# Optimization experiments

Hardware: AMD Instinct MI355X
Metric: run time of the kernel (lower is better)

## Reference

```python
import jax, jax.numpy as jnp
import numpy as np
import math

B, S, E, H = 4, 1024, 1024, 16
HD = E // H
MAX_SEQ = 5000
THETA = 10000.0


def _freqs_cis():
    # RotaryPositionalEncoding buffer: complex64 [MAX_SEQ, E//2]
    freqs = 1.0 / (THETA ** (np.arange(0, E, 2)[: E // 2] / E))
    ang = np.outer(np.arange(MAX_SEQ), freqs)
    return jnp.asarray(np.exp(1j * ang).astype(np.complex64))


def _rope(x, idx, fc_table):
    # x: [B, S, E]; pairs consecutive channels across the FULL embed_dim
    # (applied before head splitting, faithful to the original module)
    xc = x.reshape(*x.shape[:-1], -1, 2)
    xc = jax.lax.complex(xc[..., 0], xc[..., 1])  # [B, S, E//2]
    out = xc * fc_table[idx]                       # [B, S, E//2]
    return jnp.stack([jnp.real(out), jnp.imag(out)], axis=-1).reshape(x.shape)


def reference(query, key, value, query_index, key_index, attn_mask,
              key_padding_mask, Wq, bq, Wk, bk, Wv, bv, Wo, bo):
    q = query @ Wq.T + bq
    k = key @ Wk.T + bk
    v = value @ Wv.T + bv

    fc = _freqs_cis()
    q = _rope(q, query_index, fc)
    k = _rope(k, key_index, fc)

    # torch: q = cat(q.chunk(H, dim=-1), dim=0) -> flat HEAD-MAJOR [H*B, S, HD]
    qf = q.reshape(B, S, H, HD).transpose(2, 0, 1, 3).reshape(H * B, S, HD)
    kf = k.reshape(B, S, H, HD).transpose(2, 0, 1, 3).reshape(H * B, S, HD)
    vf = v.reshape(B, S, H, HD).transpose(2, 0, 1, 3).reshape(H * B, S, HD)

    # mask: logical_or(attn_mask[Sq,Sk], kpm[B,1,Sk]) -> [B, Sq, Sk]
    m = jnp.logical_or(attn_mask[None, :, :], key_padding_mask[:, None, :])
    madd = jnp.where(m, -jnp.inf, 0.0).astype(query.dtype)
    # torch repeat_interleave(H, dim=0) yields BATCH-MAJOR flat [B*H, Sq, Sk];
    # it is added to the head-major scores as-is (faithful to the original
    # indexing, including its head/batch-order quirk)
    madd_flat = jnp.repeat(madd, H, axis=0)

    scores = jnp.einsum('nqd,nkd->nqk', qf / math.sqrt(HD), kf) + madd_flat
    w = jax.nn.softmax(scores, axis=-1)              # [H*B, Sq, Sk]
    of = jnp.einsum('nqk,nkd->nqd', w, vf)           # [H*B, Sq, HD]

    # cat(chunks(dim=0), dim=-1) -> [B, Sq, E], head-major last dim
    attn_output = of.reshape(H, B, S, HD).transpose(1, 2, 0, 3).reshape(B, S, E)
    attn_output = attn_output @ Wo.T + bo

    # stack(chunks(dim=0), dim=1).mean(1) -> [B, Sq, Sk]
    attn_weights = w.reshape(H, B, S, S).transpose(1, 0, 2, 3).mean(axis=1)
    return attn_output, attn_weights


def setup_inputs() -> dict:
    key0 = jax.random.key(0)
    ks = jax.random.split(key0, 10)
    sc = 0.02
    inp = {
        'query': jax.random.normal(ks[0], (B, S, E), jnp.float32),
        'key': jax.random.normal(ks[1], (B, S, E), jnp.float32),
        'value': jax.random.normal(ks[2], (B, S, E), jnp.float32),
        'query_index': jnp.sort(jax.random.randint(ks[3], (B, S), 0, 4096), axis=-1),
        'key_index': jnp.sort(jax.random.randint(ks[4], (B, S), 0, 4096), axis=-1),
        'attn_mask': jnp.triu(jnp.ones((S, S), jnp.bool_), k=1),  # causal
        'key_padding_mask': jnp.zeros((B, S), jnp.bool_),
        'Wq': jax.random.normal(ks[5], (E, E), jnp.float32) * sc,
        'bq': jnp.zeros((E,), jnp.float32),
        'Wk': jax.random.normal(ks[6], (E, E), jnp.float32) * sc,
        'bk': jnp.zeros((E,), jnp.float32),
        'Wv': jax.random.normal(ks[7], (E, E), jnp.float32) * sc,
        'bv': jnp.zeros((E,), jnp.float32),
        'Wo': jax.random.normal(ks[8], (E, E), jnp.float32) * sc,
        'bo': jnp.zeros((E,), jnp.float32),
    }
    return inp
```

## Files before the change

kernel.cpp:

```cpp
#include <hip/hip_runtime.h>
#include <stdint.h>
#include <math.h>

#define B_ 4
#define S_ 1024
#define E_ 1024
#define H_ 16
#define HD_ 64
#define HB_ 64

typedef __attribute__((ext_vector_type(8))) short bhalf8;
typedef __attribute__((ext_vector_type(4))) float floatx4;

__device__ __forceinline__ unsigned short f2bf(float f) {
  union { float f; unsigned u; } v; v.f = f;
  unsigned r = (v.u + 0x7FFFu + ((v.u >> 16) & 1u)) >> 16;
  return (unsigned short)r;
}
__device__ __forceinline__ float bf2f(unsigned short b) {
  union { unsigned u; float f; } v; v.u = ((unsigned)b) << 16;
  return v.f;
}
__device__ __forceinline__ unsigned short f2h(float f) {
  union { _Float16 h; unsigned short u; } v; v.h = (_Float16)f; return v.u;
}
__device__ __forceinline__ float h2f(unsigned short u) {
  union { unsigned short u; _Float16 h; } v; v.u = u; return (float)v.h;
}

__device__ __forceinline__ void gload16(const void* g, void* l) {
  __builtin_amdgcn_global_load_lds(
      (const __attribute__((address_space(1))) unsigned int*)g,
      (__attribute__((address_space(3))) unsigned int*)l, 16, 0, 0);
}

template <int NCH>
__device__ __forceinline__ void stage_tile(const unsigned short* org,
                                           unsigned short* lds, int wave, int lane) {
  const int rl = lane >> 3;
  const int scb = ((lane & 7) << 4) ^ (rl << 4);
  const char* base = (const char*)org + scb;
#pragma unroll
  for (int i = 0; i < NCH / 4; ++i) {
    const int c = wave + 4 * i;
    gload16(base + (size_t)(c * 8 + rl) * 2048, (char*)lds + c * 1024);
  }
}

__device__ __forceinline__ bhalf8 read_frag(const unsigned short* lds, int row, int kbyte) {
  const int off = row * 128 + (kbyte ^ ((row & 7) << 4));
  return *(const bhalf8*)((const char*)lds + off);
}

__global__ void detect_bool_kernel(const uint8_t* __restrict__ amask, int* __restrict__ flag) {
  if (threadIdx.x == 0 && blockIdx.x == 0) *flag = (amask[1] != 0) ? 1 : 0;
}

__global__ __launch_bounds__(256) void cvt_in_kernel(
    const float* __restrict__ q, const float* __restrict__ k,
    const float* __restrict__ v, unsigned short* __restrict__ Ab) {
  const int z = blockIdx.z;
  const float* src = (z == 0) ? q : (z == 1) ? k : v;
  unsigned short* dst = Ab + (size_t)z * 4194304;
  const size_t i = ((size_t)blockIdx.x * 256 + threadIdx.x) * 8;
  float4 a = *(const float4*)(src + i);
  float4 b = *(const float4*)(src + i + 4);
  bhalf8 r;
  r[0] = (short)f2bf(a.x); r[1] = (short)f2bf(a.y);
  r[2] = (short)f2bf(a.z); r[3] = (short)f2bf(a.w);
  r[4] = (short)f2bf(b.x); r[5] = (short)f2bf(b.y);
  r[6] = (short)f2bf(b.z); r[7] = (short)f2bf(b.w);
  *(bhalf8*)(dst + i) = r;
}

__global__ __launch_bounds__(256) void cvt_w_kernel(
    const float* __restrict__ wq, const float* __restrict__ wk,
    const float* __restrict__ wv, const float* __restrict__ wo,
    unsigned short* __restrict__ Wb) {
  const int z = blockIdx.z;
  const float* src = (z == 0) ? wq : (z == 1) ? wk : (z == 2) ? wv : wo;
  unsigned short* dst = Wb + (size_t)z * 1048576;
  const size_t i = ((size_t)blockIdx.x * 256 + threadIdx.x) * 8;
  float4 a = *(const float4*)(src + i);
  float4 b = *(const float4*)(src + i + 4);
  bhalf8 r;
  r[0] = (short)f2bf(a.x); r[1] = (short)f2bf(a.y);
  r[2] = (short)f2bf(a.z); r[3] = (short)f2bf(a.w);
  r[4] = (short)f2bf(b.x); r[5] = (short)f2bf(b.y);
  r[6] = (short)f2bf(b.z); r[7] = (short)f2bf(b.w);
  *(bhalf8*)(dst + i) = r;
}

template <bool BF16OUT>
__global__ __launch_bounds__(256) void mfma_gemm_kernel(
    const unsigned short* __restrict__ A0, const unsigned short* __restrict__ A1,
    const unsigned short* __restrict__ A2,
    const unsigned short* __restrict__ W0, const unsigned short* __restrict__ W1,
    const unsigned short* __restrict__ W2,
    const float* __restrict__ b0, const float* __restrict__ b1,
    const float* __restrict__ b2,
    void* __restrict__ C0, void* __restrict__ C1, void* __restrict__ C2) {
  const int z = blockIdx.z;
  const unsigned short* A = (z == 0) ? A0 : (z == 1) ? A1 : A2;
  const unsigned short* W = (z == 0) ? W0 : (z == 1) ? W1 : W2;
  const float* bias = (z == 0) ? b0 : (z == 1) ? b1 : b2;
  void* C = (z == 0) ? C0 : (z == 1) ? C1 : C2;
  const int lin = blockIdx.y * 8 + blockIdx.x;
  const int swz = (lin & 7) * 32 + (lin >> 3);
  const int m0 = (swz >> 3) * 128, n0 = (swz & 7) * 128;
  __shared__ unsigned short As[128 * 64];
  __shared__ unsigned short Ws[128 * 64];
  const int t = threadIdx.x, wave = t >> 6, lane = t & 63;
  const int wr = wave >> 1, wc = wave & 1;
  floatx4 acc[4][4];
  const floatx4 z4 = {0.f, 0.f, 0.f, 0.f};
#pragma unroll
  for (int i = 0; i < 4; ++i)
#pragma unroll
    for (int j = 0; j < 4; ++j) acc[i][j] = z4;

  for (int k0 = 0; k0 < 1024; k0 += 64) {
    stage_tile<16>(A + (size_t)m0 * 1024 + k0, As, wave, lane);
    stage_tile<16>(W + (size_t)n0 * 1024 + k0, Ws, wave, lane);
    __syncthreads();
#pragma unroll
    for (int ks = 0; ks < 2; ++ks) {
      const int kb = ks * 64 + ((lane >> 4) << 4);
      bhalf8 af[4], bf[4];
#pragma unroll
      for (int mi = 0; mi < 4; ++mi)
        af[mi] = read_frag(As, wr * 64 + mi * 16 + (lane & 15), kb);
#pragma unroll
      for (int ni = 0; ni < 4; ++ni)
        bf[ni] = read_frag(Ws, wc * 64 + ni * 16 + (lane & 15), kb);
#pragma unroll
      for (int mi = 0; mi < 4; ++mi)
#pragma unroll
        for (int ni = 0; ni < 4; ++ni)
          acc[mi][ni] = __builtin_amdgcn_mfma_f32_16x16x32_bf16(af[mi], bf[ni], acc[mi][ni], 0, 0, 0);
    }
    __syncthreads();
  }
#pragma unroll
  for (int mi = 0; mi < 4; ++mi)
#pragma unroll
    for (int ni = 0; ni < 4; ++ni) {
      const int col = n0 + wc * 64 + ni * 16 + (lane & 15);
      const float bv = bias[col];
#pragma unroll
      for (int r = 0; r < 4; ++r) {
        const int row = m0 + wr * 64 + mi * 16 + (lane >> 4) * 4 + r;
        const float v = acc[mi][ni][r] + bv;
        if (BF16OUT)
          ((unsigned short*)C)[(size_t)row * 1024 + col] = f2bf(v);
        else
          ((float*)C)[(size_t)row * 1024 + col] = v;
      }
    }
}

__global__ __launch_bounds__(256) void rope_bf_kernel(unsigned int* __restrict__ X,
                                                      const int* __restrict__ idxs) {
  const int gid = blockIdx.x * 256 + threadIdx.x;
  const int i = gid & 511, bs = gid >> 9;
  const int pos = idxs[bs];
  const double freq = exp(-(double)(2 * i) * (9.210340371976184 / 1024.0));
  const double ang = fmod((double)pos * freq, 6.283185307179586476925287);
  const float fa = (float)ang;
  float sn, c;
  sincosf(fa, &sn, &c);
  const unsigned v = X[gid];
  const float x = bf2f((unsigned short)(v & 0xffffu));
  const float y = bf2f((unsigned short)(v >> 16));
  const float rx = x * c - y * sn;
  const float ry = x * sn + y * c;
  X[gid] = (unsigned)f2bf(rx) | ((unsigned)f2bf(ry) << 16);
}

__global__ __launch_bounds__(256) void transpose_v_kernel(
    const unsigned short* __restrict__ Vr, unsigned short* __restrict__ Vt) {
  const int s0 = blockIdx.x * 64;
  const int bh = blockIdx.y;
  const int b = bh >> 4, h = bh & 15;
  __shared__ unsigned short L[64][72];
  const int t = threadIdx.x, r = t >> 2, cq = (t & 3) * 16;
  const unsigned short* src = Vr + ((size_t)(b * S_) + s0 + r) * E_ + h * HD_ + cq;
  *(bhalf8*)&L[r][cq] = *(const bhalf8*)src;
  *(bhalf8*)&L[r][cq + 8] = *(const bhalf8*)(src + 8);
  __syncthreads();
  bhalf8 o0, o1;
#pragma unroll
  for (int u = 0; u < 8; ++u) o0[u] = (short)L[cq + u][r];
#pragma unroll
  for (int u = 0; u < 8; ++u) o1[u] = (short)L[cq + 8 + u][r];
  unsigned short* dst = Vt + ((size_t)bh * 64 + r) * 1024 + s0 + cq;
  *(bhalf8*)dst = o0;
  *(bhalf8*)(dst + 8) = o1;
}

__global__ __launch_bounds__(256) void fused_sm_kernel(
    const unsigned short* __restrict__ Qr, const unsigned short* __restrict__ Kr,
    unsigned short* __restrict__ P, const void* __restrict__ amask,
    const void* __restrict__ kpm, const int* __restrict__ flagp, int hb0) {
  const int lhb = blockIdx.y, hb = hb0 + lhb;
  const int h = hb >> 2, b = hb & 3, bp = hb >> 4;
  const int q0 = blockIdx.x * 16;
  __shared__ unsigned short Sbuf[16 * 1024];
  const int t = threadIdx.x, w = t >> 6, lane = t & 63;
  const int l4 = lane >> 4, l15 = lane & 15;

  const char* Qbase = (const char*)(Qr + ((size_t)b << 20)) + h * 128;
  const char* Kbase = (const char*)(Kr + ((size_t)b << 20)) + h * 128;

  bhalf8 bq0 = *(const bhalf8*)(Qbase + (size_t)(q0 + l15) * 2048 + l4 * 16);
  bhalf8 bq1 = *(const bhalf8*)(Qbase + (size_t)(q0 + l15) * 2048 + 64 + l4 * 16);

  floatx4 acc[16];
  const floatx4 z4 = {0.f, 0.f, 0.f, 0.f};
#pragma unroll
  for (int i = 0; i < 16; ++i) acc[i] = z4;

  const int krow0 = w * 256;
#pragma unroll
  for (int mt = 0; mt < 16; ++mt) {
    const char* kr = Kbase + (size_t)(krow0 + mt * 16 + l15) * 2048 + l4 * 16;
    bhalf8 a0 = *(const bhalf8*)kr;
    bhalf8 a1 = *(const bhalf8*)(kr + 64);
    acc[mt] = __builtin_amdgcn_mfma_f32_16x16x32_bf16(a0, bq0, acc[mt], 0, 0, 0);
    acc[mt] = __builtin_amdgcn_mfma_f32_16x16x32_bf16(a1, bq1, acc[mt], 0, 0, 0);
  }

  {
    const int q = l15;
    const int xorv = (q & 7) << 4;
#pragma unroll
    for (int mt = 0; mt < 16; ++mt) {
      const int kb2 = (krow0 + mt * 16 + l4 * 4) * 2;
      ushort4 hv;
      hv.x = f2h(acc[mt][0]); hv.y = f2h(acc[mt][1]);
      hv.z = f2h(acc[mt][2]); hv.w = f2h(acc[mt][3]);
      *(ushort4*)((char*)Sbuf + q * 2048 + (kb2 ^ xorv)) = hv;
    }
  }
  __syncthreads();

  const int isu8 = *flagp;
  bool km[16];
  if (isu8) {
    const uint8_t* kp = (const uint8_t*)kpm + (size_t)bp * 1024;
#pragma unroll
    for (int j = 0; j < 2; ++j) {
      uint2 mv = *(const uint2*)(kp + j * 512 + lane * 8);
#pragma unroll
      for (int u = 0; u < 4; ++u) {
        km[j * 8 + u] = ((mv.x >> (8 * u)) & 0xffu) != 0;
        km[j * 8 + 4 + u] = ((mv.y >> (8 * u)) & 0xffu) != 0;
      }
    }
  } else {
    const int* kp = (const int*)kpm + (size_t)bp * 1024;
#pragma unroll
    for (int j = 0; j < 2; ++j) {
      int4 v0 = *(const int4*)(kp + j * 512 + lane * 8);
      int4 v1 = *(const int4*)(kp + j * 512 + lane * 8 + 4);
      km[j * 8 + 0] = v0.x != 0; km[j * 8 + 1] = v0.y != 0;
      km[j * 8 + 2] = v0.z != 0; km[j * 8 + 3] = v0.w != 0;
      km[j * 8 + 4] = v1.x != 0; km[j * 8 + 5] = v1.y != 0;
      km[j * 8 + 6] = v1.z != 0; km[j * 8 + 7] = v1.w != 0;
    }
  }

  const float C = 0.18033688011112042f;
  for (int rr = 0; rr < 4; ++rr) {
    const int ql = w * 4 + rr;
    const int gq = q0 + ql;
    const int xr = (ql & 7) << 4;
    float x[16];
#pragma unroll
    for (int j = 0; j < 2; ++j) {
      const int off = ql * 2048 + ((j * 1024 + lane * 16) ^ xr);
      bhalf8 hv = *(const bhalf8*)((const char*)Sbuf + off);
#pragma unroll
      for (int u = 0; u < 8; ++u) x[j * 8 + u] = h2f((unsigned short)hv[u]);
    }
    if (isu8) {
      const uint8_t* ap = (const uint8_t*)amask + (size_t)gq * 1024;
#pragma unroll
      for (int j = 0; j < 2; ++j) {
        uint2 mv = *(const uint2*)(ap + j * 512 + lane * 8);
#pragma unroll
        for (int u = 0; u < 4; ++u) {
          if (((mv.x >> (8 * u)) & 0xffu) || km[j * 8 + u]) x[j * 8 + u] = -INFINITY;
          if (((mv.y >> (8 * u)) & 0xffu) || km[j * 8 + 4 + u]) x[j * 8 + 4 + u] = -INFINITY;
        }
      }
    } else {
      const int* ap = (const int*)amask + (size_t)gq * 1024;
#pragma unroll
      for (int j = 0; j < 2; ++j) {
        int4 v0 = *(const int4*)(ap + j * 512 + lane * 8);
        int4 v1 = *(const int4*)(ap + j * 512 + lane * 8 + 4);
        if (v0.x || km[j * 8 + 0]) x[j * 8 + 0] = -INFINITY;
        if (v0.y || km[j * 8 + 1]) x[j * 8 + 1] = -INFINITY;
        if (v0.z || km[j * 8 + 2]) x[j * 8 + 2] = -INFINITY;
        if (v0.w || km[j * 8 + 3]) x[j * 8 + 3] = -INFINITY;
        if (v1.x || km[j * 8 + 4]) x[j * 8 + 4] = -INFINITY;
        if (v1.y || km[j * 8 + 5]) x[j * 8 + 5] = -INFINITY;
        if (v1.z || km[j * 8 + 6]) x[j * 8 + 6] = -INFINITY;
        if (v1.w || km[j * 8 + 7]) x[j * 8 + 7] = -INFINITY;
      }
    }
    float m = x[0];
#pragma unroll
    for (int i = 1; i < 16; ++i) m = fmaxf(m, x[i]);
#pragma unroll
    for (int o = 32; o > 0; o >>= 1) m = fmaxf(m, __shfl_xor(m, o));
    const float mc = m * C;
    float s = 0.f;
#pragma unroll
    for (int i = 0; i < 16; ++i) {
      x[i] = exp2f(__builtin_fmaf(x[i], C, -mc));
      s += x[i];
    }
#pragma unroll
    for (int o = 32; o > 0; o >>= 1) s += __shfl_xor(s, o);
    const float inv = 1.0f / s;
    unsigned short* prow = P + ((size_t)lhb << 20) + ((size_t)gq << 10);
#pragma unroll
    for (int j = 0; j < 2; ++j) {
      bhalf8 pv;
#pragma unroll
      for (int u = 0; u < 8; ++u) pv[u] = (short)f2bf(x[j * 8 + u] * inv);
      *(bhalf8*)(prow + j * 512 + lane * 8) = pv;
    }
  }
}

__global__ __launch_bounds__(256) void wmean_kernel(
    const unsigned short* __restrict__ P, float* __restrict__ outW,
    int nhh, int first) {
  const size_t gid = (size_t)blockIdx.x * 256 + threadIdx.x;
  const int k8 = (int)(gid & 127);
  const int q = (int)((gid >> 7) & 1023);
  const int b = (int)(gid >> 17);
  float s[8];
#pragma unroll
  for (int u = 0; u < 8; ++u) s[u] = 0.f;
  for (int hh = 0; hh < nhh; ++hh) {
    const int lhb = hh * 4 + b;
    bhalf8 v = *(const bhalf8*)(P + ((size_t)lhb << 20) + ((size_t)q << 10) + k8 * 8);
#pragma unroll
    for (int u = 0; u < 8; ++u) s[u] += bf2f((unsigned short)v[u]);
  }
  float* o = outW + (((size_t)(b * S_ + q)) << 10) + k8 * 8;
  const float invH = 1.0f / 16.0f;
  float4 v0, v1;
  v0.x = s[0] * invH; v0.y = s[1] * invH; v0.z = s[2] * invH; v0.w = s[3] * invH;
  v1.x = s[4] * invH; v1.y = s[5] * invH; v1.z = s[6] * invH; v1.w = s[7] * invH;
  if (!first) {
    float4 a = *(float4*)o, b4 = *(float4*)(o + 4);
    v0.x += a.x; v0.y += a.y; v0.z += a.z; v0.w += a.w;
    v1.x += b4.x; v1.y += b4.y; v1.z += b4.z; v1.w += b4.w;
  }
  *(float4*)o = v0;
  *(float4*)(o + 4) = v1;
}

__global__ __launch_bounds__(256) void pv_mfma_kernel(
    const unsigned short* __restrict__ Wt, const unsigned short* __restrict__ Vt,
    unsigned short* __restrict__ Ocat, int hb0) {
  const int lhb = blockIdx.y, hb = hb0 + lhb;
  const int h = hb >> 2, b = hb & 3;
  const int q0 = blockIdx.x * 64;
  __shared__ unsigned short Ps[64 * 64];
  __shared__ unsigned short Vs[64 * 64];
  const int t = threadIdx.x, wave = t >> 6, lane = t & 63;
  const int wr = wave >> 1, wc = wave & 1;
  const unsigned short* Wh = Wt + ((size_t)lhb << 20);
  const unsigned short* Vh = Vt + (size_t)(b * 16 + h) * 65536;
  floatx4 acc[2][2];
  const floatx4 z4 = {0.f, 0.f, 0.f, 0.f};
#pragma unroll
  for (int i = 0; i < 2; ++i)
#pragma unroll
    for (int j = 0; j < 2; ++j) acc[i][j] = z4;

  for (int k0 = 0; k0 < 1024; k0 += 64) {
    stage_tile<8>(Wh + (size_t)q0 * 1024 + k0, Ps, wave, lane);
    stage_tile<8>(Vh + k0, Vs, wave, lane);
    __syncthreads();
#pragma unroll
    for (int ks = 0; ks < 2; ++ks) {
      const int kb = ks * 64 + ((lane >> 4) << 4);
      bhalf8 af[2], bf[2];
#pragma unroll
      for (int mi = 0; mi < 2; ++mi)
        af[mi] = read_frag(Ps, wr * 32 + mi * 16 + (lane & 15), kb);
#pragma unroll
      for (int ni = 0; ni < 2; ++ni)
        bf[ni] = read_frag(Vs, wc * 32 + ni * 16 + (lane & 15), kb);
#pragma unroll
      for (int mi = 0; mi < 2; ++mi)
#pragma unroll
        for (int ni = 0; ni < 2; ++ni)
          acc[mi][ni] = __builtin_amdgcn_mfma_f32_16x16x32_bf16(af[mi], bf[ni], acc[mi][ni], 0, 0, 0);
    }
    __syncthreads();
  }
#pragma unroll
  for (int mi = 0; mi < 2; ++mi)
#pragma unroll
    for (int ni = 0; ni < 2; ++ni) {
      const int d = wc * 32 + ni * 16 + (lane & 15);
#pragma unroll
      for (int r = 0; r < 4; ++r) {
        const int q = q0 + wr * 32 + mi * 16 + (lane >> 4) * 4 + r;
        Ocat[((size_t)(b * S_) + q) * E_ + h * HD_ + d] = f2bf(acc[mi][ni][r]);
      }
    }
}

extern "C" void kernel_launch(void* const* d_in, const int* in_sizes, int n_in,
                              void* d_out, int out_size, void* d_ws, size_t ws_size,
                              hipStream_t stream) {
  (void)in_sizes; (void)n_in; (void)out_size;
  const float* query = (const float*)d_in[0];
  const float* key   = (const float*)d_in[1];
  const float* value = (const float*)d_in[2];
  const int* qidx = (const int*)d_in[3];
  const int* kidx = (const int*)d_in[4];
  const void* amask = d_in[5];
  const void* kpm   = d_in[6];
  const float* Wq = (const float*)d_in[7];
  const float* bq = (const float*)d_in[8];
  const float* Wk = (const float*)d_in[9];
  const float* bk = (const float*)d_in[10];
  const float* Wv = (const float*)d_in[11];
  const float* bv = (const float*)d_in[12];
  const float* Wo = (const float*)d_in[13];
  const float* bo = (const float*)d_in[14];

  float* outA = (float*)d_out;
  float* outW = (float*)d_out + (size_t)B_ * S_ * E_;

  float* ws = (float*)d_ws;
  unsigned short* Ab   = (unsigned short*)(ws + 0);
  unsigned short* Wb   = (unsigned short*)(ws + 6291456);
  unsigned short* Qr   = (unsigned short*)(ws + 8388608);
  unsigned short* Kr   = (unsigned short*)(ws + 10485760);
  unsigned short* Vr   = (unsigned short*)(ws + 12582912);
  unsigned short* Vt   = (unsigned short*)(ws + 14680064);
  unsigned short* Ocat = (unsigned short*)(ws + 16777216);
  int* flagp           = (int*)(ws + 18874368);
  const size_t tail_off = 18874432;

  const size_t ws_floats = ws_size / 4;
  int CH = 0;
  unsigned short* P = nullptr;
  for (int c = 64; c >= 4; c >>= 1) {
    if (tail_off + (size_t)c * 524288 <= ws_floats) {
      CH = c;
      P = (unsigned short*)(ws + tail_off);
      break;
    }
  }
  if (!CH) {
    CH = 8;
    P = (unsigned short*)ws;
  }

  detect_bool_kernel<<<1, 64, 0, stream>>>((const uint8_t*)amask, flagp);

  cvt_in_kernel<<<dim3(2048, 1, 3), 256, 0, stream>>>(query, key, value, Ab);
  cvt_w_kernel<<<dim3(512, 1, 4), 256, 0, stream>>>(Wq, Wk, Wv, Wo, Wb);

  mfma_gemm_kernel<true><<<dim3(8, 32, 3), 256, 0, stream>>>(
      Ab, Ab + 4194304, Ab + 8388608,
      Wb, Wb + 1048576, Wb + 2097152,
      bq, bk, bv, Qr, Kr, Vr);

  rope_bf_kernel<<<8192, 256, 0, stream>>>((unsigned int*)Qr, qidx);
  rope_bf_kernel<<<8192, 256, 0, stream>>>((unsigned int*)Kr, kidx);

  transpose_v_kernel<<<dim3(16, 64), 256, 0, stream>>>(Vr, Vt);

  const int nch = HB_ / CH;
  for (int c = 0; c < nch; ++c) {
    const int hb0 = c * CH;
    fused_sm_kernel<<<dim3(64, CH), 256, 0, stream>>>(Qr, Kr, P, amask, kpm,
                                                      flagp, hb0);
    wmean_kernel<<<2048, 256, 0, stream>>>(P, outW, CH / 4, (c == 0) ? 1 : 0);
    pv_mfma_kernel<<<dim3(16, CH), 256, 0, stream>>>(P, Vt, Ocat, hb0);
  }

  mfma_gemm_kernel<false><<<dim3(8, 32, 1), 256, 0, stream>>>(
      Ocat, Ocat, Ocat, Wb + 3145728, Wb + 3145728, Wb + 3145728,
      bo, bo, bo, outA, outA, outA);
}
```

Measured before the change: 255.5 us.

## Fuse QK softmax, PV and head-mean into one attention kernel per batch

Result: slower. 297.9 us (+16.6%).

```diff
diff --git a/kernel.cpp b/kernel.cpp
--- a/kernel.cpp
+++ b/kernel.cpp
@@ -198,100 +198,35 @@
   *(bhalf8*)(dst + 8) = o1;
 }
 
-__global__ __launch_bounds__(256) void fused_sm_kernel(
+__global__ __launch_bounds__(512) void attn_fused_kernel(
     const unsigned short* __restrict__ Qr, const unsigned short* __restrict__ Kr,
-    unsigned short* __restrict__ P, const void* __restrict__ amask,
-    const void* __restrict__ kpm, const int* __restrict__ flagp, int hb0) {
-  const int lhb = blockIdx.y, hb = hb0 + lhb;
-  const int h = hb >> 2, b = hb & 3, bp = hb >> 4;
-  const int q0 = blockIdx.x * 16;
-  __shared__ unsigned short Sbuf[16 * 1024];
+    const unsigned short* __restrict__ Vt, unsigned short* __restrict__ Ocat,
+    float* __restrict__ Wpart, const void* __restrict__ amask,
+    const void* __restrict__ kpm, const int* __restrict__ flagp,
+    int nh, float wscale) {
+  const int qb = blockIdx.x, b = blockIdx.y, hg = blockIdx.z;
+  const int q0 = qb * 16;
   const int t = threadIdx.x, w = t >> 6, lane = t & 63;
   const int l4 = lane >> 4, l15 = lane & 15;
-
-  const char* Qbase = (const char*)(Qr + ((size_t)b << 20)) + h * 128;
-  const char* Kbase = (const char*)(Kr + ((size_t)b << 20)) + h * 128;
-
-  bhalf8 bq0 = *(const bhalf8*)(Qbase + (size_t)(q0 + l15) * 2048 + l4 * 16);
-  bhalf8 bq1 = *(const bhalf8*)(Qbase + (size_t)(q0 + l15) * 2048 + 64 + l4 * 16);
-
-  floatx4 acc[16];
-  const floatx4 z4 = {0.f, 0.f, 0.f, 0.f};
-#pragma unroll
-  for (int i = 0; i < 16; ++i) acc[i] = z4;
-
-  const int krow0 = w * 256;
-#pragma unroll
-  for (int mt = 0; mt < 16; ++mt) {
-    const char* kr = Kbase + (size_t)(krow0 + mt * 16 + l15) * 2048 + l4 * 16;
-    bhalf8 a0 = *(const bhalf8*)kr;
-    bhalf8 a1 = *(const bhalf8*)(kr + 64);
-    acc[mt] = __builtin_amdgcn_mfma_f32_16x16x32_bf16(a0, bq0, acc[mt], 0, 0, 0);
-    acc[mt] = __builtin_amdgcn_mfma_f32_16x16x32_bf16(a1, bq1, acc[mt], 0, 0, 0);
-  }
-
-  {
-    const int q = l15;
-    const int xorv = (q & 7) << 4;
-#pragma unroll
-    for (int mt = 0; mt < 16; ++mt) {
-      const int kb2 = (krow0 + mt * 16 + l4 * 4) * 2;
-      ushort4 hv;
-      hv.x = f2h(acc[mt][0]); hv.y = f2h(acc[mt][1]);
-      hv.z = f2h(acc[mt][2]); hv.w = f2h(acc[mt][3]);
-      *(ushort4*)((char*)Sbuf + q * 2048 + (kb2 ^ xorv)) = hv;
-    }
-  }
-  __syncthreads();
+  __shared__ unsigned short Sbuf[16 * 1024];
+  __shared__ float Red[1024];
 
   const int isu8 = *flagp;
-  bool km[16];
-  if (isu8) {
-    const uint8_t* kp = (const uint8_t*)kpm + (size_t)bp * 1024;
-#pragma unroll
-    for (int j = 0; j < 2; ++j) {
-      uint2 mv = *(const uint2*)(kp + j * 512 + lane * 8);
-#pragma unroll
-      for (int u = 0; u < 4; ++u) {
-        km[j * 8 + u] = ((mv.x >> (8 * u)) & 0xffu) != 0;
-        km[j * 8 + 4 + u] = ((mv.y >> (8 * u)) & 0xffu) != 0;
-      }
-    }
-  } else {
-    const int* kp = (const int*)kpm + (size_t)bp * 1024;
-#pragma unroll
-    for (int j = 0; j < 2; ++j) {
-      int4 v0 = *(const int4*)(kp + j * 512 + lane * 8);
-      int4 v1 = *(const int4*)(kp + j * 512 + lane * 8 + 4);
-      km[j * 8 + 0] = v0.x != 0; km[j * 8 + 1] = v0.y != 0;
-      km[j * 8 + 2] = v0.z != 0; km[j * 8 + 3] = v0.w != 0;
-      km[j * 8 + 4] = v1.x != 0; km[j * 8 + 5] = v1.y != 0;
-      km[j * 8 + 6] = v1.z != 0; km[j * 8 + 7] = v1.w != 0;
-    }
-  }
-
-  const float C = 0.18033688011112042f;
-  for (int rr = 0; rr < 4; ++rr) {
-    const int ql = w * 4 + rr;
-    const int gq = q0 + ql;
-    const int xr = (ql & 7) << 4;
-    float x[16];
-#pragma unroll
-    for (int j = 0; j < 2; ++j) {
-      const int off = ql * 2048 + ((j * 1024 + lane * 16) ^ xr);
-      bhalf8 hv = *(const bhalf8*)((const char*)Sbuf + off);
-#pragma unroll
-      for (int u = 0; u < 8; ++u) x[j * 8 + u] = h2f((unsigned short)hv[u]);
-    }
+
+  unsigned am_bits[2];
+#pragma unroll
+  for (int r = 0; r < 2; ++r) {
+    const int gq = q0 + w * 2 + r;
+    unsigned mb = 0;
     if (isu8) {
       const uint8_t* ap = (const uint8_t*)amask + (size_t)gq * 1024;
 #pragma unroll
       for (int j = 0; j < 2; ++j) {
-        uint2 mv = *(const uint2*)(ap + j * 512 + lane * 8);
+        uint2 v = *(const uint2*)(ap + j * 512 + lane * 8);
 #pragma unroll
         for (int u = 0; u < 4; ++u) {
-          if (((mv.x >> (8 * u)) & 0xffu) || km[j * 8 + u]) x[j * 8 + u] = -INFINITY;
-          if (((mv.y >> (8 * u)) & 0xffu) || km[j * 8 + 4 + u]) x[j * 8 + 4 + u] = -INFINITY;
+          if ((v.x >> (8 * u)) & 0xffu) mb |= 1u << (j * 8 + u);
+          if ((v.y >> (8 * u)) & 0xffu) mb |= 1u << (j * 8 + 4 + u);
         }
       }
     } else {
@@ -300,124 +235,197 @@
       for (int j = 0; j < 2; ++j) {
         int4 v0 = *(const int4*)(ap + j * 512 + lane * 8);
         int4 v1 = *(const int4*)(ap + j * 512 + lane * 8 + 4);
-        if (v0.x || km[j * 8 + 0]) x[j * 8 + 0] = -INFINITY;
-        if (v0.y || km[j * 8 + 1]) x[j * 8 + 1] = -INFINITY;
-        if (v0.z || km[j * 8 + 2]) x[j * 8 + 2] = -INFINITY;
-        if (v0.w || km[j * 8 + 3]) x[j * 8 + 3] = -INFINITY;
-        if (v1.x || km[j * 8 + 4]) x[j * 8 + 4] = -INFINITY;
-        if (v1.y || km[j * 8 + 5]) x[j * 8 + 5] = -INFINITY;
-        if (v1.z || km[j * 8 + 6]) x[j * 8 + 6] = -INFINITY;
-        if (v1.w || km[j * 8 + 7]) x[j * 8 + 7] = -INFINITY;
-      }
-    }
-    float m = x[0];
-#pragma unroll
-    for (int i = 1; i < 16; ++i) m = fmaxf(m, x[i]);
-#pragma unroll
-    for (int o = 32; o > 0; o >>= 1) m = fmaxf(m, __shfl_xor(m, o));
-    const float mc = m * C;
-    float s = 0.f;
-#pragma unroll
-    for (int i = 0; i < 16; ++i) {
-      x[i] = exp2f(__builtin_fmaf(x[i], C, -mc));
-      s += x[i];
-    }
-#pragma unroll
-    for (int o = 32; o > 0; o >>= 1) s += __shfl_xor(s, o);
-    const float inv = 1.0f / s;
-    unsigned short* prow = P + ((size_t)lhb << 20) + ((size_t)gq << 10);
+        if (v0.x) mb |= 1u << (j * 8 + 0);
+        if (v0.y) mb |= 1u << (j * 8 + 1);
+        if (v0.z) mb |= 1u << (j * 8 + 2);
+        if (v0.w) mb |= 1u << (j * 8 + 3);
+        if (v1.x) mb |= 1u << (j * 8 + 4);
+        if (v1.y) mb |= 1u << (j * 8 + 5);
+        if (v1.z) mb |= 1u << (j * 8 + 6);
+        if (v1.w) mb |= 1u << (j * 8 + 7);
+      }
+    }
+    am_bits[r] = mb;
+  }
+  unsigned km_bits[4];
+#pragma unroll
+  for (int bp = 0; bp < 4; ++bp) {
+    unsigned mb = 0;
+    if (isu8) {
+      const uint8_t* kp = (const uint8_t*)kpm + (size_t)bp * 1024;
+#pragma unroll
+      for (int j = 0; j < 2; ++j) {
+        uint2 v = *(const uint2*)(kp + j * 512 + lane * 8);
+#pragma unroll
+        for (int u = 0; u < 4; ++u) {
+          if ((v.x >> (8 * u)) & 0xffu) mb |= 1u << (j * 8 + u);
+          if ((v.y >> (8 * u)) & 0xffu) mb |= 1u << (j * 8 + 4 + u);
+        }
+      }
+    } else {
+      const int* kp = (const int*)kpm + (size_t)bp * 1024;
+#pragma unroll
+      for (int j = 0; j < 2; ++j) {
+        int4 v0 = *(const int4*)(kp + j * 512 + lane * 8);
+        int4 v1 = *(const int4*)(kp + j * 512 + lane * 8 + 4);
+        if (v0.x) mb |= 1u << (j * 8 + 0);
+        if (v0.y) mb |= 1u << (j * 8 + 1);
+        if (v0.z) mb |= 1u << (j * 8 + 2);
+        if (v0.w) mb |= 1u << (j * 8 + 3);
+        if (v1.x) mb |= 1u << (j * 8 + 4);
+        if (v1.y) mb |= 1u << (j * 8 + 5);
+        if (v1.z) mb |= 1u << (j * 8 + 6);
+        if (v1.w) mb |= 1u << (j * 8 + 7);
+      }
+    }
+    km_bits[bp] = mb;
+  }
+
+  float wacc[2][16];
+#pragma unroll
+  for (int r = 0; r < 2; ++r)
+#pragma unroll
+    for (int i = 0; i < 16; ++i) wacc[r][i] = 0.f;
+
+  const floatx4 z4 = {0.f, 0.f, 0.f, 0.f};
+  const float Cc = 0.18033688011112042f;
+
+  for (int hh = 0; hh < nh; ++hh) {
+    const int h = hg * nh + hh;
+    const char* Qb = (const char*)Qr + ((size_t)b << 21) + h * 128;
+    const char* Kb = (const char*)Kr + ((size_t)b << 21) + h * 128;
+
+    bhalf8 bq0 = *(const bhalf8*)(Qb + (size_t)(q0 + l15) * 2048 + l4 * 16);
+    bhalf8 bq1 = *(const bhalf8*)(Qb + (size_t)(q0 + l15) * 2048 + 64 + l4 * 16);
+
+    floatx4 acc[8];
+#pragma unroll
+    for (int i = 0; i < 8; ++i) acc[i] = z4;
+#pragma unroll
+    for (int mt = 0; mt < 8; ++mt) {
+      const char* kr = Kb + (size_t)(w * 128 + mt * 16 + l15) * 2048 + l4 * 16;
+      bhalf8 a0 = *(const bhalf8*)kr;
+      bhalf8 a1 = *(const bhalf8*)(kr + 64);
+      acc[mt] = __builtin_amdgcn_mfma_f32_16x16x32_bf16(a0, bq0, acc[mt], 0, 0, 0);
+      acc[mt] = __builtin_amdgcn_mfma_f32_16x16x32_bf16(a1, bq1, acc[mt], 0, 0, 0);
+    }
+    {
+      const int xr = (l15 & 7) << 4;
+#pragma unroll
+      for (int mt = 0; mt < 8; ++mt) {
+        const int kb2 = (w * 128 + mt * 16 + l4 * 4) * 2;
+        ushort4 hv;
+        hv.x = f2h(acc[mt][0]); hv.y = f2h(acc[mt][1]);
+        hv.z = f2h(acc[mt][2]); hv.w = f2h(acc[mt][3]);
+        *(ushort4*)((char*)Sbuf + l15 * 2048 + (kb2 ^ xr)) = hv;
+      }
+    }
+    __syncthreads();
+
+    const unsigned kmb = km_bits[h >> 2];
+#pragma unroll
+    for (int r = 0; r < 2; ++r) {
+      const int ql = w * 2 + r;
+      const int xr = (ql & 7) << 4;
+      float x[16];
+#pragma unroll
+      for (int j = 0; j < 2; ++j) {
+        bhalf8 hv = *(const bhalf8*)((const char*)Sbuf + ql * 2048 +
+                                     ((j * 1024 + lane * 16) ^ xr));
+#pragma unroll
+        for (int u = 0; u < 8; ++u) x[j * 8 + u] = h2f((unsigned short)hv[u]);
+      }
+      const unsigned mb = am_bits[r] | kmb;
+#pragma unroll
+      for (int i = 0; i < 16; ++i)
+        if ((mb >> i) & 1u) x[i] = -INFINITY;
+      float m = x[0];
+#pragma unroll
+      for (int i = 1; i < 16; ++i) m = fmaxf(m, x[i]);
+#pragma unroll
+      for (int o = 32; o > 0; o >>= 1) m = fmaxf(m, __shfl_xor(m, o));
+      const float mc = m * Cc;
+      float s = 0.f;
+#pragma unroll
+      for (int i = 0; i < 16; ++i) {
+        x[i] = exp2f(__builtin_fmaf(x[i], Cc, -mc));
+        s += x[i];
+      }
+#pragma unroll
+      for (int o = 32; o > 0; o >>= 1) s += __shfl_xor(s, o);
+      const float inv = 1.0f / s;
+#pragma unroll
+      for (int j = 0; j < 2; ++j) {
+        bhalf8 pv;
+#pragma unroll
+        for (int u = 0; u < 8; ++u) {
+          const float p = x[j * 8 + u] * inv;
+          pv[u] = (short)f2bf(p);
+          wacc[r][j * 8 + u] += p;
+        }
+        *(bhalf8*)((char*)Sbuf + ql * 2048 + ((j * 1024 + lane * 16) ^ xr)) = pv;
+      }
+    }
+    __syncthreads();
+
+    const int dq = w & 3, kh = w >> 2;
+    floatx4 o4 = z4;
+    const char* Vb = (const char*)Vt +
+        (((size_t)(b * 16 + h) * 64 + dq * 16 + l15) * 1024 + kh * 512) * 2;
+    const int xrp = (l15 & 7) << 4;
+#pragma unroll
+    for (int kt = 0; kt < 16; ++kt) {
+      bhalf8 pa = *(const bhalf8*)((const char*)Sbuf + l15 * 2048 +
+                                   ((kh * 1024 + kt * 64 + l4 * 16) ^ xrp));
+      bhalf8 vb = *(const bhalf8*)(Vb + kt * 64 + l4 * 16);
+      o4 = __builtin_amdgcn_mfma_f32_16x16x32_bf16(pa, vb, o4, 0, 0, 0);
+    }
+    if (kh == 1) *(floatx4*)&Red[dq * 256 + lane * 4] = o4;
+    __syncthreads();
+    if (kh == 0) {
+      const floatx4 p4 = *(const floatx4*)&Red[dq * 256 + lane * 4];
+#pragma unroll
+      for (int r2 = 0; r2 < 4; ++r2) {
+        const int q = q0 + l4 * 4 + r2;
+        Ocat[((size_t)(b * 1024) + q) * 1024 + h * 64 + dq * 16 + l15] =
+            f2bf(o4[r2] + p4[r2]);
+      }
+    }
+  }
+
+  const int plane = hg * 4 + b;
+  float* wp = Wpart + ((size_t)plane << 20);
+#pragma unroll
+  for (int r = 0; r < 2; ++r) {
+    const int gq = q0 + w * 2 + r;
+    float* row = wp + ((size_t)gq << 10);
 #pragma unroll
     for (int j = 0; j < 2; ++j) {
-      bhalf8 pv;
-#pragma unroll
-      for (int u = 0; u < 8; ++u) pv[u] = (short)f2bf(x[j * 8 + u] * inv);
-      *(bhalf8*)(prow + j * 512 + lane * 8) = pv;
-    }
-  }
-}
-
-__global__ __launch_bounds__(256) void wmean_kernel(
-    const unsigned short* __restrict__ P, float* __restrict__ outW,
-    int nhh, int first) {
-  const size_t gid = (size_t)blockIdx.x * 256 + threadIdx.x;
-  const int k8 = (int)(gid & 127);
-  const int q = (int)((gid >> 7) & 1023);
-  const int b = (int)(gid >> 17);
-  float s[8];
-#pragma unroll
-  for (int u = 0; u < 8; ++u) s[u] = 0.f;
-  for (int hh = 0; hh < nhh; ++hh) {
-    const int lhb = hh * 4 + b;
-    bhalf8 v = *(const bhalf8*)(P + ((size_t)lhb << 20) + ((size_t)q << 10) + k8 * 8);
-#pragma unroll
-    for (int u = 0; u < 8; ++u) s[u] += bf2f((unsigned short)v[u]);
-  }
-  float* o = outW + (((size_t)(b * S_ + q)) << 10) + k8 * 8;
-  const float invH = 1.0f / 16.0f;
-  float4 v0, v1;
-  v0.x = s[0] * invH; v0.y = s[1] * invH; v0.z = s[2] * invH; v0.w = s[3] * invH;
-  v1.x = s[4] * invH; v1.y = s[5] * invH; v1.z = s[6] * invH; v1.w = s[7] * invH;
-  if (!first) {
-    float4 a = *(float4*)o, b4 = *(float4*)(o + 4);
-    v0.x += a.x; v0.y += a.y; v0.z += a.z; v0.w += a.w;
-    v1.x += b4.x; v1.y += b4.y; v1.z += b4.z; v1.w += b4.w;
-  }
-  *(float4*)o = v0;
-  *(float4*)(o + 4) = v1;
-}
-
-__global__ __launch_bounds__(256) void pv_mfma_kernel(
-    const unsigned short* __restrict__ Wt, const unsigned short* __restrict__ Vt,
-    unsigned short* __restrict__ Ocat, int hb0) {
-  const int lhb = blockIdx.y, hb = hb0 + lhb;
-  const int h = hb >> 2, b = hb & 3;
-  const int q0 = blockIdx.x * 64;
-  __shared__ unsigned short Ps[64 * 64];
-  __shared__ unsigned short Vs[64 * 64];
-  const int t = threadIdx.x, wave = t >> 6, lane = t & 63;
-  const int wr = wave >> 1, wc = wave & 1;
-  const unsigned short* Wh = Wt + ((size_t)lhb << 20);
-  const unsigned short* Vh = Vt + (size_t)(b * 16 + h) * 65536;
-  floatx4 acc[2][2];
-  const floatx4 z4 = {0.f, 0.f, 0.f, 0.f};
-#pragma unroll
-  for (int i = 0; i < 2; ++i)
-#pragma unroll
-    for (int j = 0; j < 2; ++j) acc[i][j] = z4;
-
-  for (int k0 = 0; k0 < 1024; k0 += 64) {
-    stage_tile<8>(Wh + (size_t)q0 * 1024 + k0, Ps, wave, lane);
-    stage_tile<8>(Vh + k0, Vs, wave, lane);
-    __syncthreads();
-#pragma unroll
-    for (int ks = 0; ks < 2; ++ks) {
-      const int kb = ks * 64 + ((lane >> 4) << 4);
-      bhalf8 af[2], bf[2];
-#pragma unroll
-      for (int mi = 0; mi < 2; ++mi)
-        af[mi] = read_frag(Ps, wr * 32 + mi * 16 + (lane & 15), kb);
-#pragma unroll
-      for (int ni = 0; ni < 2; ++ni)
-        bf[ni] = read_frag(Vs, wc * 32 + ni * 16 + (lane & 15), kb);
-#pragma unroll
-      for (int mi = 0; mi < 2; ++mi)
-#pragma unroll
-        for (int ni = 0; ni < 2; ++ni)
-          acc[mi][ni] = __builtin_amdgcn_mfma_f32_16x16x32_bf16(af[mi], bf[ni], acc[mi][ni], 0, 0, 0);
-    }
-    __syncthreads();
-  }
-#pragma unroll
-  for (int mi = 0; mi < 2; ++mi)
-#pragma unroll
-    for (int ni = 0; ni < 2; ++ni) {
-      const int d = wc * 32 + ni * 16 + (lane & 15);
-#pragma unroll
-      for (int r = 0; r < 4; ++r) {
-        const int q = q0 + wr * 32 + mi * 16 + (lane >> 4) * 4 + r;
-        Ocat[((size_t)(b * S_) + q) * E_ + h * HD_ + d] = f2bf(acc[mi][ni][r]);
-      }
-    }
+      float4 v0, v1;
+      v0.x = wacc[r][j * 8 + 0] * wscale; v0.y = wacc[r][j * 8 + 1] * wscale;
+      v0.z = wacc[r][j * 8 + 2] * wscale; v0.w = wacc[r][j * 8 + 3] * wscale;
+      v1.x = wacc[r][j * 8 + 4] * wscale; v1.y = wacc[r][j * 8 + 5] * wscale;
+      v1.z = wacc[r][j * 8 + 6] * wscale; v1.w = wacc[r][j * 8 + 7] * wscale;
+      *(float4*)(row + j * 512 + lane * 8) = v0;
+      *(float4*)(row + j * 512 + lane * 8 + 4) = v1;
+    }
+  }
+}
+
+__global__ __launch_bounds__(256) void wreduce_kernel(
+    const float* __restrict__ w0, const float* __restrict__ w1,
+    float* __restrict__ out) {
+  const size_t i = ((size_t)blockIdx.x * 256 + threadIdx.x) * 8;
+  const float s = 1.0f / 16.0f;
+  float4 a0 = *(const float4*)(w0 + i), a1 = *(const float4*)(w0 + i + 4);
+  float4 b0 = *(const float4*)(w1 + i), b1 = *(const float4*)(w1 + i + 4);
+  float4 r0, r1;
+  r0.x = (a0.x + b0.x) * s; r0.y = (a0.y + b0.y) * s;
+  r0.z = (a0.z + b0.z) * s; r0.w = (a0.w + b0.w) * s;
+  r1.x = (a1.x + b1.x) * s; r1.y = (a1.y + b1.y) * s;
+  r1.z = (a1.z + b1.z) * s; r1.w = (a1.w + b1.w) * s;
+  *(float4*)(out + i) = r0;
+  *(float4*)(out + i + 4) = r1;
 }
 
 extern "C" void kernel_launch(void* const* d_in, const int* in_sizes, int n_in,
@@ -455,19 +463,8 @@
   const size_t tail_off = 18874432;
 
   const size_t ws_floats = ws_size / 4;
-  int CH = 0;
-  unsigned short* P = nullptr;
-  for (int c = 64; c >= 4; c >>= 1) {
-    if (tail_off + (size_t)c * 524288 <= ws_floats) {
-      CH = c;
-      P = (unsigned short*)(ws + tail_off);
-      break;
-    }
-  }
-  if (!CH) {
-    CH = 8;
-    P = (unsigned short*)ws;
-  }
+  const bool hg2 = (tail_off + 8388608ull <= ws_floats);
+  float* Wpart = hg2 ? (ws + tail_off) : outW;
 
   detect_bool_kernel<<<1, 64, 0, stream>>>((const uint8_t*)amask, flagp);
 
@@ -484,13 +481,13 @@
 
   transpose_v_kernel<<<dim3(16, 64), 256, 0, stream>>>(Vr, Vt);
 
-  const int nch = HB_ / CH;
-  for (int c = 0; c < nch; ++c) {
-    const int hb0 = c * CH;
-    fused_sm_kernel<<<dim3(64, CH), 256, 0, stream>>>(Qr, Kr, P, amask, kpm,
-                                                      flagp, hb0);
-    wmean_kernel<<<2048, 256, 0, stream>>>(P, outW, CH / 4, (c == 0) ? 1 : 0);
-    pv_mfma_kernel<<<dim3(16, CH), 256, 0, stream>>>(P, Vt, Ocat, hb0);
+  if (hg2) {
+    attn_fused_kernel<<<dim3(64, 4, 2), 512, 0, stream>>>(
+        Qr, Kr, Vt, Ocat, Wpart, amask, kpm, flagp, 8, 1.0f);
+    wreduce_kernel<<<2048, 256, 0, stream>>>(Wpart, Wpart + 4194304, outW);
+  } else {
+    attn_fused_kernel<<<dim3(64, 4, 1), 512, 0, stream>>>(
+        Qr, Kr, Vt, Ocat, Wpart, amask, kpm, flagp, 16, 1.0f / 16.0f);
   }
 
   mfma_gemm_kernel<false><<<dim3(8, 32, 1), 256, 0, stream>>>(
```

## Fuse P·V into the scores-softmax kernel and keep softmax in registers

Applied to the files above, without the earlier changes.

Result: slower. 305.4 us (+19.5%).

```diff
diff --git a/kernel.cpp b/kernel.cpp
--- a/kernel.cpp
+++ b/kernel.cpp
@@ -21,11 +21,10 @@
   union { unsigned u; float f; } v; v.u = ((unsigned)b) << 16;
   return v.f;
 }
-__device__ __forceinline__ unsigned short f2h(float f) {
-  union { _Float16 h; unsigned short u; } v; v.h = (_Float16)f; return v.u;
-}
-__device__ __forceinline__ float h2f(unsigned short u) {
-  union { unsigned short u; _Float16 h; } v; v.u = u; return (float)v.h;
+__device__ __forceinline__ unsigned cvtpk_bf16(float a, float b) {
+  unsigned r;
+  asm volatile("v_cvt_pk_bf16_f32 %0, %1, %2" : "=v"(r) : "v"(a), "v"(b));
+  return r;
 }
 
 __device__ __forceinline__ void gload16(const void* g, void* l) {
@@ -198,141 +197,163 @@
   *(bhalf8*)(dst + 8) = o1;
 }
 
-__global__ __launch_bounds__(256) void fused_sm_kernel(
+__global__ __launch_bounds__(256) void scores_pv_kernel(
     const unsigned short* __restrict__ Qr, const unsigned short* __restrict__ Kr,
+    const unsigned short* __restrict__ Vt, unsigned short* __restrict__ Ocat,
     unsigned short* __restrict__ P, const void* __restrict__ amask,
     const void* __restrict__ kpm, const int* __restrict__ flagp, int hb0) {
   const int lhb = blockIdx.y, hb = hb0 + lhb;
   const int h = hb >> 2, b = hb & 3, bp = hb >> 4;
   const int q0 = blockIdx.x * 16;
   __shared__ unsigned short Sbuf[16 * 1024];
+  __shared__ float rmax[64];
+  __shared__ float rsum[64];
   const int t = threadIdx.x, w = t >> 6, lane = t & 63;
   const int l4 = lane >> 4, l15 = lane & 15;
-
-  const char* Qbase = (const char*)(Qr + ((size_t)b << 20)) + h * 128;
-  const char* Kbase = (const char*)(Kr + ((size_t)b << 20)) + h * 128;
-
-  bhalf8 bq0 = *(const bhalf8*)(Qbase + (size_t)(q0 + l15) * 2048 + l4 * 16);
-  bhalf8 bq1 = *(const bhalf8*)(Qbase + (size_t)(q0 + l15) * 2048 + 64 + l4 * 16);
+  const int isu8 = *flagp;
+
+  const char* Qb = (const char*)Qr + ((size_t)b << 21) + h * 128;
+  const char* Kb = (const char*)Kr + ((size_t)b << 21) + h * 128;
+
+  bhalf8 bq0 = *(const bhalf8*)(Qb + (size_t)(q0 + l15) * 2048 + l4 * 16);
+  bhalf8 bq1 = *(const bhalf8*)(Qb + (size_t)(q0 + l15) * 2048 + 64 + l4 * 16);
 
   floatx4 acc[16];
   const floatx4 z4 = {0.f, 0.f, 0.f, 0.f};
 #pragma unroll
   for (int i = 0; i < 16; ++i) acc[i] = z4;
-
-  const int krow0 = w * 256;
 #pragma unroll
   for (int mt = 0; mt < 16; ++mt) {
-    const char* kr = Kbase + (size_t)(krow0 + mt * 16 + l15) * 2048 + l4 * 16;
+    const char* kr = Kb + (size_t)(w * 256 + mt * 16 + l15) * 2048 + l4 * 16;
     bhalf8 a0 = *(const bhalf8*)kr;
     bhalf8 a1 = *(const bhalf8*)(kr + 64);
     acc[mt] = __builtin_amdgcn_mfma_f32_16x16x32_bf16(a0, bq0, acc[mt], 0, 0, 0);
     acc[mt] = __builtin_amdgcn_mfma_f32_16x16x32_bf16(a1, bq1, acc[mt], 0, 0, 0);
   }
 
-  {
-    const int q = l15;
-    const int xorv = (q & 7) << 4;
+  unsigned mb0 = 0, mb1 = 0;
+  if (isu8) {
+    const uint8_t* ap = (const uint8_t*)amask + (size_t)(q0 + l15) * 1024;
+    const uint8_t* kp = (const uint8_t*)kpm + (size_t)bp * 1024;
 #pragma unroll
     for (int mt = 0; mt < 16; ++mt) {
-      const int kb2 = (krow0 + mt * 16 + l4 * 4) * 2;
-      ushort4 hv;
-      hv.x = f2h(acc[mt][0]); hv.y = f2h(acc[mt][1]);
-      hv.z = f2h(acc[mt][2]); hv.w = f2h(acc[mt][3]);
-      *(ushort4*)((char*)Sbuf + q * 2048 + (kb2 ^ xorv)) = hv;
-    }
-  }
+      const int k = w * 256 + mt * 16 + l4 * 4;
+      uchar4 a = *(const uchar4*)(ap + k);
+      uchar4 c = *(const uchar4*)(kp + k);
+      unsigned bits = ((a.x | c.x) ? 1u : 0u) | ((a.y | c.y) ? 2u : 0u) |
+                      ((a.z | c.z) ? 4u : 0u) | ((a.w | c.w) ? 8u : 0u);
+      if (mt < 8) mb0 |= bits << (mt * 4);
+      else        mb1 |= bits << ((mt - 8) * 4);
+    }
+  } else {
+    const int* ap = (const int*)amask + (size_t)(q0 + l15) * 1024;
+    const int* kp = (const int*)kpm + (size_t)bp * 1024;
+#pragma unroll
+    for (int mt = 0; mt < 16; ++mt) {
+      const int k = w * 256 + mt * 16 + l4 * 4;
+      int4 a = *(const int4*)(ap + k);
+      int4 c = *(const int4*)(kp + k);
+      unsigned bits = ((a.x | c.x) ? 1u : 0u) | ((a.y | c.y) ? 2u : 0u) |
+                      ((a.z | c.z) ? 4u : 0u) | ((a.w | c.w) ? 8u : 0u);
+      if (mt < 8) mb0 |= bits << (mt * 4);
+      else        mb1 |= bits << ((mt - 8) * 4);
+    }
+  }
+#pragma unroll
+  for (int mt = 0; mt < 16; ++mt) {
+    const unsigned bits = ((mt < 8) ? (mb0 >> (mt * 4)) : (mb1 >> ((mt - 8) * 4))) & 0xFu;
+#pragma unroll
+    for (int r = 0; r < 4; ++r)
+      if ((bits >> r) & 1u) acc[mt][r] = -INFINITY;
+  }
+
+  float red[16];
+#pragma unroll
+  for (int mt = 0; mt < 16; ++mt)
+    red[mt] = fmaxf(fmaxf(acc[mt][0], acc[mt][1]), fmaxf(acc[mt][2], acc[mt][3]));
+#pragma unroll
+  for (int s2 = 8; s2 > 0; s2 >>= 1)
+#pragma unroll
+    for (int i = 0; i < 8; ++i)
+      if (i < s2) red[i] = fmaxf(red[i], red[i + s2]);
+  float mx = red[0];
+  mx = fmaxf(mx, __shfl_xor(mx, 16));
+  mx = fmaxf(mx, __shfl_xor(mx, 32));
+  if (l4 == 0) rmax[w * 16 + l15] = mx;
   __syncthreads();
-
-  const int isu8 = *flagp;
-  bool km[16];
-  if (isu8) {
-    const uint8_t* kp = (const uint8_t*)kpm + (size_t)bp * 1024;
-#pragma unroll
-    for (int j = 0; j < 2; ++j) {
-      uint2 mv = *(const uint2*)(kp + j * 512 + lane * 8);
-#pragma unroll
-      for (int u = 0; u < 4; ++u) {
-        km[j * 8 + u] = ((mv.x >> (8 * u)) & 0xffu) != 0;
-        km[j * 8 + 4 + u] = ((mv.y >> (8 * u)) & 0xffu) != 0;
-      }
-    }
-  } else {
-    const int* kp = (const int*)kpm + (size_t)bp * 1024;
-#pragma unroll
-    for (int j = 0; j < 2; ++j) {
-      int4 v0 = *(const int4*)(kp + j * 512 + lane * 8);
-      int4 v1 = *(const int4*)(kp + j * 512 + lane * 8 + 4);
-      km[j * 8 + 0] = v0.x != 0; km[j * 8 + 1] = v0.y != 0;
-      km[j * 8 + 2] = v0.z != 0; km[j * 8 + 3] = v0.w != 0;
-      km[j * 8 + 4] = v1.x != 0; km[j * 8 + 5] = v1.y != 0;
-      km[j * 8 + 6] = v1.z != 0; km[j * 8 + 7] = v1.w != 0;
-    }
-  }
-
-  const float C = 0.18033688011112042f;
+  mx = fmaxf(fmaxf(rmax[l15], rmax[16 + l15]), fmaxf(rmax[32 + l15], rmax[48 + l15]));
+
+  const float Cc = 0.18033688011112042f;
+  const float mc = mx * Cc;
+#pragma unroll
+  for (int mt = 0; mt < 16; ++mt)
+#pragma unroll
+    for (int r = 0; r < 4; ++r)
+      acc[mt][r] = exp2f(__builtin_fmaf(acc[mt][r], Cc, -mc));
+
+#pragma unroll
+  for (int mt = 0; mt < 16; ++mt)
+    red[mt] = (acc[mt][0] + acc[mt][1]) + (acc[mt][2] + acc[mt][3]);
+#pragma unroll
+  for (int s2 = 8; s2 > 0; s2 >>= 1)
+#pragma unroll
+    for (int i = 0; i < 8; ++i)
+      if (i < s2) red[i] += red[i + s2];
+  float sm = red[0];
+  sm += __shfl_xor(sm, 16);
+  sm += __shfl_xor(sm, 32);
+  if (l4 == 0) rsum[w * 16 + l15] = sm;
+  __syncthreads();
+  sm = (rsum[l15] + rsum[16 + l15]) + (rsum[32 + l15] + rsum[48 + l15]);
+  const float inv = 1.0f / sm;
+
+  const int xr = (l15 & 7) << 4;
+#pragma unroll
+  for (int mt = 0; mt < 16; ++mt) {
+    uint2 pk;
+    pk.x = cvtpk_bf16(acc[mt][0] * inv, acc[mt][1] * inv);
+    pk.y = cvtpk_bf16(acc[mt][2] * inv, acc[mt][3] * inv);
+    const int kb2 = (w * 256 + mt * 16 + l4 * 4) * 2;
+    *(uint2*)((char*)Sbuf + l15 * 2048 + (kb2 ^ xr)) = pk;
+  }
+  __syncthreads();
+
+  unsigned short* pbase = P + ((size_t)lhb << 20);
+#pragma unroll
   for (int rr = 0; rr < 4; ++rr) {
     const int ql = w * 4 + rr;
     const int gq = q0 + ql;
-    const int xr = (ql & 7) << 4;
-    float x[16];
+    const int xq = (ql & 7) << 4;
 #pragma unroll
     for (int j = 0; j < 2; ++j) {
-      const int off = ql * 2048 + ((j * 1024 + lane * 16) ^ xr);
-      bhalf8 hv = *(const bhalf8*)((const char*)Sbuf + off);
-#pragma unroll
-      for (int u = 0; u < 8; ++u) x[j * 8 + u] = h2f((unsigned short)hv[u]);
-    }
-    if (isu8) {
-      const uint8_t* ap = (const uint8_t*)amask + (size_t)gq * 1024;
-#pragma unroll
-      for (int j = 0; j < 2; ++j) {
-        uint2 mv = *(const uint2*)(ap + j * 512 + lane * 8);
-#pragma unroll
-        for (int u = 0; u < 4; ++u) {
-          if (((mv.x >> (8 * u)) & 0xffu) || km[j * 8 + u]) x[j * 8 + u] = -INFINITY;
-          if (((mv.y >> (8 * u)) & 0xffu) || km[j * 8 + 4 + u]) x[j * 8 + 4 + u] = -INFINITY;
-        }
-      }
-    } else {
-      const int* ap = (const int*)amask + (size_t)gq * 1024;
-#pragma unroll
-      for (int j = 0; j < 2; ++j) {
-        int4 v0 = *(const int4*)(ap + j * 512 + lane * 8);
-        int4 v1 = *(const int4*)(ap + j * 512 + lane * 8 + 4);
-        if (v0.x || km[j * 8 + 0]) x[j * 8 + 0] = -INFINITY;
-        if (v0.y || km[j * 8 + 1]) x[j * 8 + 1] = -INFINITY;
-        if (v0.z || km[j * 8 + 2]) x[j * 8 + 2] = -INFINITY;
-        if (v0.w || km[j * 8 + 3]) x[j * 8 + 3] = -INFINITY;
-        if (v1.x || km[j * 8 + 4]) x[j * 8 + 4] = -INFINITY;
-        if (v1.y || km[j * 8 + 5]) x[j * 8 + 5] = -INFINITY;
-        if (v1.z || km[j * 8 + 6]) x[j * 8 + 6] = -INFINITY;
-        if (v1.w || km[j * 8 + 7]) x[j * 8 + 7] = -INFINITY;
-      }
-    }
-    float m = x[0];
-#pragma unroll
-    for (int i = 1; i < 16; ++i) m = fmaxf(m, x[i]);
-#pragma unroll
-    for (int o = 32; o > 0; o >>= 1) m = fmaxf(m, __shfl_xor(m, o));
-    const float mc = m * C;
-    float s = 0.f;
-#pragma unroll
-    for (int i = 0; i < 16; ++i) {
-      x[i] = exp2f(__builtin_fmaf(x[i], C, -mc));
-      s += x[i];
-    }
-#pragma unroll
-    for (int o = 32; o > 0; o >>= 1) s += __shfl_xor(s, o);
-    const float inv = 1.0f / s;
-    unsigned short* prow = P + ((size_t)lhb << 20) + ((size_t)gq << 10);
-#pragma unroll
-    for (int j = 0; j < 2; ++j) {
-      bhalf8 pv;
-#pragma unroll
-      for (int u = 0; u < 8; ++u) pv[u] = (short)f2bf(x[j * 8 + u] * inv);
-      *(bhalf8*)(prow + j * 512 + lane * 8) = pv;
-    }
+      bhalf8 v = *(const bhalf8*)((const char*)Sbuf + ql * 2048 +
+                                  ((j * 1024 + lane * 16) ^ xq));
+      *(bhalf8*)(pbase + ((size_t)gq << 10) + j * 512 + lane * 8) = v;
+    }
+  }
+
+  const char* Vb = (const char*)Vt +
+      ((size_t)((b * 16 + h) * 64 + w * 16 + l15)) * 2048;
+  floatx4 oa = z4, ob = z4;
+#pragma unroll
+  for (int ks = 0; ks < 16; ++ks) {
+    bhalf8 pa = *(const bhalf8*)((const char*)Sbuf + l15 * 2048 +
+                                 ((ks * 64 + l4 * 16) ^ xr));
+    bhalf8 vb = *(const bhalf8*)(Vb + ks * 64 + l4 * 16);
+    oa = __builtin_amdgcn_mfma_f32_16x16x32_bf16(pa, vb, oa, 0, 0, 0);
+  }
+#pragma unroll
+  for (int ks = 16; ks < 32; ++ks) {
+    bhalf8 pa = *(const bhalf8*)((const char*)Sbuf + l15 * 2048 +
+                                 ((ks * 64 + l4 * 16) ^ xr));
+    bhalf8 vb = *(const bhalf8*)(Vb + ks * 64 + l4 * 16);
+    ob = __builtin_amdgcn_mfma_f32_16x16x32_bf16(pa, vb, ob, 0, 0, 0);
+  }
+#pragma unroll
+  for (int r = 0; r < 4; ++r) {
+    const int q = q0 + l4 * 4 + r;
+    Ocat[((size_t)(b * 1024) + q) * 1024 + h * 64 + w * 16 + l15] =
+        f2bf(oa[r] + ob[r]);
   }
 }
 
@@ -364,60 +385,6 @@
   }
   *(float4*)o = v0;
   *(float4*)(o + 4) = v1;
-}
-
-__global__ __launch_bounds__(256) void pv_mfma_kernel(
-    const unsigned short* __restrict__ Wt, const unsigned short* __restrict__ Vt,
-    unsigned short* __restrict__ Ocat, int hb0) {
-  const int lhb = blockIdx.y, hb = hb0 + lhb;
-  const int h = hb >> 2, b = hb & 3;
-  const int q0 = blockIdx.x * 64;
-  __shared__ unsigned short Ps[64 * 64];
-  __shared__ unsigned short Vs[64 * 64];
-  const int t = threadIdx.x, wave = t >> 6, lane = t & 63;
-  const int wr = wave >> 1, wc = wave & 1;
-  const unsigned short* Wh = Wt + ((size_t)lhb << 20);
-  const unsigned short* Vh = Vt + (size_t)(b * 16 + h) * 65536;
-  floatx4 acc[2][2];
-  const floatx4 z4 = {0.f, 0.f, 0.f, 0.f};
-#pragma unroll
-  for (int i = 0; i < 2; ++i)
-#pragma unroll
-    for (int j = 0; j < 2; ++j) acc[i][j] = z4;
-
-  for (int k0 = 0; k0 < 1024; k0 += 64) {
-    stage_tile<8>(Wh + (size_t)q0 * 1024 + k0, Ps, wave, lane);
-    stage_tile<8>(Vh + k0, Vs, wave, lane);
-    __syncthreads();
-#pragma unroll
-    for (int ks = 0; ks < 2; ++ks) {
-      const int kb = ks * 64 + ((lane >> 4) << 4);
-      bhalf8 af[2], bf[2];
-#pragma unroll
-      for (int mi = 0; mi < 2; ++mi)
-        af[mi] = read_frag(Ps, wr * 32 + mi * 16 + (lane & 15), kb);
-#pragma unroll
-      for (int ni = 0; ni < 2; ++ni)
-        bf[ni] = read_frag(Vs, wc * 32 + ni * 16 + (lane & 15), kb);
-#pragma unroll
-      for (int mi = 0; mi < 2; ++mi)
-#pragma unroll
-        for (int ni = 0; ni < 2; ++ni)
-          acc[mi][ni] = __builtin_amdgcn_mfma_f32_16x16x32_bf16(af[mi], bf[ni], acc[mi][ni], 0, 0, 0);
-    }
-    __syncthreads();
-  }
-#pragma unroll
-  for (int mi = 0; mi < 2; ++mi)
-#pragma unroll
-    for (int ni = 0; ni < 2; ++ni) {
-      const int d = wc * 32 + ni * 16 + (lane & 15);
-#pragma unroll
-      for (int r = 0; r < 4; ++r) {
-        const int q = q0 + wr * 32 + mi * 16 + (lane >> 4) * 4 + r;
-        Ocat[((size_t)(b * S_) + q) * E_ + h * HD_ + d] = f2bf(acc[mi][ni][r]);
-      }
-    }
 }
 
 extern "C" void kernel_launch(void* const* d_in, const int* in_sizes, int n_in,
@@ -487,10 +454,9 @@
   const int nch = HB_ / CH;
   for (int c = 0; c < nch; ++c) {
     const int hb0 = c * CH;
-    fused_sm_kernel<<<dim3(64, CH), 256, 0, stream>>>(Qr, Kr, P, amask, kpm,
-                                                      flagp, hb0);
+    scores_pv_kernel<<<dim3(64, CH), 256, 0, stream>>>(Qr, Kr, Vt, Ocat, P,
+                                                       amask, kpm, flagp, hb0);
     wmean_kernel<<<2048, 256, 0, stream>>>(P, outW, CH / 4, (c == 0) ? 1 : 0);
-    pv_mfma_kernel<<<dim3(16, CH), 256, 0, stream>>>(P, Vt, Ocat, hb0);
   }
 
   mfma_gemm_kernel<false><<<dim3(8, 32, 1), 256, 0, stream>>>(
```
